# Kernel optimization log

Measured on AMD Instinct MI355X. Metric: run time of the kernel, lower is better.

The kernel has to match this reference:

```python
import jax, jax.numpy as jnp
import numpy as np
import math

D_MODEL = 1024
NUM_HEADS = 16
SEQ = 2048
BATCH = 4


def setup_inputs() -> dict:
    key = jax.random.key(0)
    ks = jax.random.split(key, 7)
    s = 0.02
    return {
        "x": jax.random.normal(ks[0], (BATCH, SEQ, D_MODEL), jnp.float32),
        "Wq": jax.random.normal(ks[1], (D_MODEL, D_MODEL), jnp.float32) * s,
        "bq": jax.random.normal(ks[2], (D_MODEL,), jnp.float32) * s,
        "Wkv": jax.random.normal(ks[3], (D_MODEL, 2 * D_MODEL), jnp.float32) * s,
        "bkv": jax.random.normal(ks[4], (2 * D_MODEL,), jnp.float32) * s,
        "Wo": jax.random.normal(ks[5], (D_MODEL, D_MODEL), jnp.float32) * s,
        "bo": jax.random.normal(ks[6], (D_MODEL,), jnp.float32) * s,
        "decoderMask": 1,
    }


def reference(x, Wq, bq, Wkv, bkv, Wo, bo, decoderMask):
    B, S, D = x.shape
    H = NUM_HEADS
    dh = D // H
    q_ = x @ Wq + bq              # [B,S,D]
    kv_ = x @ Wkv + bkv           # [B,S,2D] (self-attention: m is None)
    # Faithful to source: concat [q_, kv_] then reshape into heads of 3*dh,
    # which interleaves Q/KV projection columns across heads.
    qkv = jnp.concatenate([q_, kv_], axis=-1)          # [B,S,3D]
    qkv = qkv.reshape(B, S, H, 3 * dh).transpose(0, 2, 1, 3)  # [B,H,S,3dh]
    q, k, v = jnp.split(qkv, 3, axis=-1)               # each [B,H,S,dh]
    scaled = jnp.einsum("bhqd,bhkd->bhqk", q, k) / math.sqrt(dh)
    if decoderMask:
        mask = jnp.triu(jnp.full((S, S), -jnp.inf, dtype=scaled.dtype), k=1)
        scaled = scaled + mask
    attn = jax.nn.softmax(scaled, axis=-1)
    vals = jnp.einsum("bhqk,bhkd->bhqd", attn, v)      # [B,H,S,dh]
    vals = vals.transpose(0, 2, 1, 3).reshape(B, S, D)
    return vals @ Wo + bo
```

## Files before the change

kernel.cpp:

```cpp
#include <hip/hip_runtime.h>
#include <cstddef>
#include <cstdint>

#define SEQ   2048
#define BATCH 4
#define DM    1024
#define NH    16
#define DH    64
#define ROWS  (BATCH*SEQ)
#define NC3   3072
#define SM_SCALE 0.18033688f

typedef unsigned short u16;
typedef __attribute__((ext_vector_type(8))) short bf16x8;
typedef __attribute__((ext_vector_type(2))) float f32x2;
typedef __attribute__((ext_vector_type(4))) float f32x4;
typedef __attribute__((ext_vector_type(16))) float f32x16;
typedef __attribute__((ext_vector_type(4))) unsigned u32x4;
typedef __attribute__((ext_vector_type(2))) unsigned u32x2;

union V16 { f32x16 v; f32x2 p[8]; };

__device__ __forceinline__ u16 f2b(float f) {
  union { float f; unsigned u; } v; v.f = f;
  unsigned r = v.u + 0x7fffu + ((v.u >> 16) & 1u);
  return (u16)(r >> 16);
}

__device__ __forceinline__ unsigned cvt_pk_bf16(float lo, float hi) {
  unsigned r;
  asm("v_cvt_pk_bf16_f32 %0, %1, %2" : "=v"(r) : "v"(lo), "v"(hi));
  return r;
}

__device__ __forceinline__ void plswap(unsigned& a, unsigned& b) {
  auto rr = __builtin_amdgcn_permlane32_swap((int)a, (int)b, false, false);
  a = (unsigned)rr[0];
  b = (unsigned)rr[1];
}

__device__ __forceinline__ float ex2(float x) { return __builtin_amdgcn_exp2f(x); }

__device__ __forceinline__ void gld16(const void* g, void* l) {
  __builtin_amdgcn_global_load_lds((const __attribute__((address_space(1))) void*)g,
                                   (__attribute__((address_space(3))) void*)l,
                                   16, 0, 0);
}

__global__ __launch_bounds__(256) void prep_tw_kernel(
    const float* __restrict__ x, const float* __restrict__ bq,
    const float* __restrict__ bkv, u16* __restrict__ xb, float* __restrict__ bc,
    const float* __restrict__ Wq, const float* __restrict__ Wkv,
    const float* __restrict__ Wo, u16* __restrict__ Wt)
{
  __shared__ float t_[32][33];
  const int tid = threadIdx.x;
  if (blockIdx.x < 8192) {
    int i = blockIdx.x * 256 + tid;
    int idx = i * 4;
    float4 v = *(const float4*)(x + idx);
    xb[idx + 0] = f2b(v.x);
    xb[idx + 1] = f2b(v.y);
    xb[idx + 2] = f2b(v.z);
    xb[idx + 3] = f2b(v.w);
    if (i < NC3) bc[i] = (i < DM) ? bq[i] : bkv[i - DM];
  } else {
    const int bid = blockIdx.x - 8192;
    const int n0 = (bid & 127) * 32, k0 = (bid >> 7) * 32;
    const int xcol = tid & 31, yrow = tid >> 5;
    #pragma unroll
    for (int it = 0; it < 4; ++it) {
      int k = k0 + yrow + it * 8;
      int n = n0 + xcol;
      float v;
      if (n < DM)           v = Wq[k * DM + n];
      else if (n < NC3)     v = Wkv[k * (2 * DM) + (n - DM)];
      else                  v = Wo[k * DM + (n - NC3)];
      t_[yrow + it * 8][xcol] = v;
    }
    __syncthreads();
    #pragma unroll
    for (int it = 0; it < 4; ++it) {
      int n = n0 + yrow + it * 8;
      int k = k0 + xcol;
      Wt[(size_t)n * DM + k] = f2b(t_[xcol][yrow + it * 8]);
    }
  }
}

template <int MODE>
__global__ __launch_bounds__(256) void gemm_bt(
    const u16* __restrict__ A, const u16* __restrict__ Bt,
    const float* __restrict__ bias, void* __restrict__ C,
    u16* __restrict__ Vt, int M, int N, int K)
{
  __shared__ alignas(16) u16 lds_[4 * 8192];
  const int tid = threadIdx.x;
  const int lane = tid & 63, wid = tid >> 6;
  const int wr = (wid >> 1) * 64, wc = (wid & 1) * 64;
  const int l15 = lane & 15, lhi = lane >> 4;
  const int row0 = blockIdx.y * 128, col0 = blockIdx.x * 128;
  const int sr = tid >> 2, scol = (tid & 3) * 8;

  const u16* aS0 = A  + (size_t)(row0 + sr) * K + scol;
  const u16* aS1 = A  + (size_t)(row0 + 64 + sr) * K + scol;
  const u16* bS0 = Bt + (size_t)(col0 + sr) * K + scol;
  const u16* bS1 = Bt + (size_t)(col0 + 64 + sr) * K + scol;
  const int dA = tid * 8;

  int aoff[4], boff[4];
  #pragma unroll
  for (int m = 0; m < 4; ++m) aoff[m] = (wr + m * 16 + l15) * 32 + lhi * 8;
  #pragma unroll
  for (int n = 0; n < 4; ++n) boff[n] = 4096 + (wc + n * 16 + l15) * 32 + lhi * 8;

  f32x4 acc[4][4];
  #pragma unroll
  for (int m = 0; m < 4; ++m)
    #pragma unroll
    for (int n = 0; n < 4; ++n) { f32x4 z = {0.f, 0.f, 0.f, 0.f}; acc[m][n] = z; }

  const int KT = K >> 5;

  auto stage = [&](int kt) {
    u16* base = lds_ + (kt & 3) * 8192;
    const int ka = kt * 32;
    gld16(aS0 + ka, base + dA);
    gld16(aS1 + ka, base + 2048 + dA);
    gld16(bS0 + ka, base + 4096 + dA);
    gld16(bS1 + ka, base + 6144 + dA);
  };

  stage(0); stage(1); stage(2);
  asm volatile("s_waitcnt vmcnt(8)" ::: "memory");
  __builtin_amdgcn_s_barrier();

  for (int kt = 0; kt < KT; ++kt) {
    const u16* buf = lds_ + (kt & 3) * 8192;
    bf16x8 a[4], b[4];
    #pragma unroll
    for (int m = 0; m < 4; ++m) a[m] = *(const bf16x8*)&buf[aoff[m]];
    #pragma unroll
    for (int n = 0; n < 4; ++n) b[n] = *(const bf16x8*)&buf[boff[n]];
    if (kt + 3 < KT) stage(kt + 3);
    __builtin_amdgcn_s_setprio(1);
    #pragma unroll
    for (int m = 0; m < 4; ++m)
      #pragma unroll
      for (int n = 0; n < 4; ++n)
        acc[m][n] = __builtin_amdgcn_mfma_f32_16x16x32_bf16(a[m], b[n], acc[m][n], 0, 0, 0);
    __builtin_amdgcn_s_setprio(0);
    if (kt + 3 < KT)      { asm volatile("s_waitcnt vmcnt(8)" ::: "memory"); }
    else if (kt + 2 < KT) { asm volatile("s_waitcnt vmcnt(4)" ::: "memory"); }
    else if (kt + 1 < KT) { asm volatile("s_waitcnt vmcnt(0)" ::: "memory"); }
    __builtin_amdgcn_s_barrier();
  }

  #pragma unroll
  for (int m = 0; m < 4; ++m)
    #pragma unroll
    for (int n = 0; n < 4; ++n) {
      const int col = col0 + wc + n * 16 + l15;
      const float bv = bias[col];
      if (MODE == 0) {
        #pragma unroll
        for (int r = 0; r < 4; ++r) {
          const int row = row0 + wr + m * 16 + lhi * 4 + r;
          ((float*)C)[(size_t)row * N + col] = acc[m][n][r] + bv;
        }
      } else {
        const int hh = col / 192;
        const int cc = col - hh * 192;
        const float qs = (cc < 64) ? SM_SCALE : 1.f;
        u16 wv[4];
        #pragma unroll
        for (int r = 0; r < 4; ++r) {
          const int row = row0 + wr + m * 16 + lhi * 4 + r;
          wv[r] = f2b((acc[m][n][r] + bv) * qs);
          ((u16*)C)[(size_t)row * N + col] = wv[r];
        }
        if (cc >= 128) {
          const int row = row0 + wr + m * 16 + lhi * 4;
          const int bb = row >> 11, j = row & (SEQ - 1);
          u16* vt = Vt + ((size_t)(bb * NH + hh) * 64 + (cc - 128)) * SEQ + j;
          u32x2 pv = { (unsigned)wv[0] | ((unsigned)wv[1] << 16),
                       (unsigned)wv[2] | ((unsigned)wv[3] << 16) };
          *(u32x2*)vt = pv;
        }
      }
    }
}

__global__ __launch_bounds__(256) void attn_kernel(
    const u16* __restrict__ qkv, const u16* __restrict__ Vt, u16* __restrict__ ctx)
{
  const int bid = blockIdx.x;
  const int p   = (bid >> 3) & 7;
  const int g   = (bid & 7) + ((bid >> 6) << 3);
  const int h   = g & 15, b = g >> 4;
  const int tid = threadIdx.x;
  const int lane = tid & 63, wid = tid >> 6;
  const int l31 = lane & 31, lhi5 = lane >> 5;

  __shared__ alignas(16) u16 smem[4 * 64 * 64];

  const size_t kv_row = (size_t)(b * NH + h) * 64;
  const int sr = tid >> 3, sck = tid & 7;
  const int scks = sck ^ (sr & 7);

  const u16* kSrc0 = qkv + (size_t)(b * SEQ + sr) * NC3 + h * 192 + 64 + scks * 8;
  const u16* kSrc1 = kSrc0 + (size_t)32 * NC3;
  const u16* vSrc0 = Vt + (kv_row + sr) * SEQ + scks * 8;
  const u16* vSrc1 = vSrc0 + (size_t)32 * SEQ;
  const int dOff0 = sr * 64 + sck * 8;
  const int dOff1 = (32 + sr) * 64 + sck * 8;

  int koff[4], koff2[4];
  #pragma unroll
  for (int c = 0; c < 4; ++c) {
    koff[c]  = l31 * 64        + (((2 * c + lhi5) ^ (l31 & 7)) * 8);
    koff2[c] = (32 + l31) * 64 + (((2 * c + lhi5) ^ (l31 & 7)) * 8);
  }

  #pragma unroll 1
  for (int half = 0; half < 2; ++half) {
    const int qt = half ? (7 - p) : (8 + p);
    const int q0 = qt * 128;

    #pragma unroll
    for (int it = 0; it < 4; ++it) {
      int row = it * 32 + sr;
      gld16(qkv + (size_t)(b * SEQ + q0 + row) * NC3 + h * 192 + scks * 8,
            &smem[row * 64 + sck * 8]);
    }
    gld16(kSrc0, &smem[8192 + dOff0]);
    gld16(kSrc1, &smem[8192 + dOff1]);
    gld16(vSrc0, &smem[12288 + dOff0]);
    gld16(vSrc1, &smem[12288 + dOff1]);
    __syncthreads();

    bf16x8 qf[4];
    {
      const int qrow = wid * 32 + l31;
      #pragma unroll
      for (int c = 0; c < 4; ++c)
        qf[c] = *(const bf16x8*)&smem[qrow * 64 + (((2 * c + lhi5) ^ (qrow & 7)) * 8)];
    }
    __syncthreads();

    V16 o0, o1;
    #pragma unroll
    for (int r = 0; r < 16; ++r) { o0.v[r] = 0.f; o1.v[r] = 0.f; }
    float lrow = 0.f;

    const int nt = qt * 2 + 2;
    const int qw0 = q0 + wid * 32;
    const int qa  = qw0 + l31;
    const int dqb = qa - 4 * lhi5;

    for (int jt = 0; jt < nt; ++jt) {
      const int j0 = jt * 64;
      const u16* Kb = smem + ((jt & 1) ? 0 : 8192);
      const u16* Vb = smem + ((jt & 1) ? 4096 : 12288);

      if (jt + 1 < nt) {
        u16* Kn = smem + ((jt & 1) ? 8192 : 0);
        u16* Vn = smem + ((jt & 1) ? 12288 : 4096);
        const size_t kAdv = (size_t)(j0 + 64) * NC3;
        const int    vAdv = j0 + 64;
        gld16(kSrc0 + kAdv, &Kn[dOff0]);
        gld16(kSrc1 + kAdv, &Kn[dOff1]);
        gld16(vSrc0 + vAdv, &Vn[dOff0]);
        gld16(vSrc1 + vAdv, &Vn[dOff1]);
      }

      if (j0 <= qw0 + 31) {
        V16 s0, s1;
        #pragma unroll
        for (int r = 0; r < 16; ++r) { s0.v[r] = 0.f; s1.v[r] = 0.f; }
        __builtin_amdgcn_s_setprio(1);
        #pragma unroll
        for (int c = 0; c < 4; ++c) {
          bf16x8 kf = *(const bf16x8*)&Kb[koff[c]];
          s0.v = __builtin_amdgcn_mfma_f32_32x32x16_bf16(kf, qf[c], s0.v, 0, 0, 0);
        }
        #pragma unroll
        for (int c = 0; c < 4; ++c) {
          bf16x8 kf = *(const bf16x8*)&Kb[koff2[c]];
          s1.v = __builtin_amdgcn_mfma_f32_32x32x16_bf16(kf, qf[c], s1.v, 0, 0, 0);
        }
        __builtin_amdgcn_s_setprio(0);

        if (j0 + 63 > qw0) {
          const int dq = dqb - j0;
          #pragma unroll
          for (int r = 0; r < 16; ++r) {
            const int kvc = (r & 3) + 8 * (r >> 2);
            s0.v[r] = (kvc > dq)      ? -1e30f : s0.v[r];
            s1.v[r] = (kvc + 32 > dq) ? -1e30f : s1.v[r];
          }
        }

        f32x2 sum2 = {0.f, 0.f};
        #pragma unroll
        for (int i = 0; i < 8; ++i) {
          f32x2 e0, e1;
          e0[0] = ex2(s0.p[i][0]); e0[1] = ex2(s0.p[i][1]);
          e1[0] = ex2(s1.p[i][0]); e1[1] = ex2(s1.p[i][1]);
          s0.p[i] = e0; s1.p[i] = e1;
          sum2 += e0 + e1;
        }
        float ps = sum2[0] + sum2[1];
        {
          unsigned a = __builtin_bit_cast(unsigned, ps), bb = a;
          plswap(a, bb);
          ps = __builtin_bit_cast(float, a) + __builtin_bit_cast(float, bb);
        }
        lrow += ps;

        unsigned pk0[8], pk1[8];
        #pragma unroll
        for (int i = 0; i < 4; ++i) {
          pk0[2 * i]     = cvt_pk_bf16(s0.v[4 * i + 0], s0.v[4 * i + 1]);
          pk0[2 * i + 1] = cvt_pk_bf16(s0.v[4 * i + 2], s0.v[4 * i + 3]);
          pk1[2 * i]     = cvt_pk_bf16(s1.v[4 * i + 0], s1.v[4 * i + 1]);
          pk1[2 * i + 1] = cvt_pk_bf16(s1.v[4 * i + 2], s1.v[4 * i + 3]);
        }
        bf16x8 pf[4];
        {
          unsigned a0 = pk0[0], b0 = pk0[2]; plswap(a0, b0);
          unsigned a1 = pk0[1], b1 = pk0[3]; plswap(a1, b1);
          u32x4 w0v = {a0, a1, b0, b1}; pf[0] = __builtin_bit_cast(bf16x8, w0v);
          unsigned a2 = pk0[4], b2 = pk0[6]; plswap(a2, b2);
          unsigned a3 = pk0[5], b3 = pk0[7]; plswap(a3, b3);
          u32x4 w1v = {a2, a3, b2, b3}; pf[1] = __builtin_bit_cast(bf16x8, w1v);
          unsigned a4 = pk1[0], b4 = pk1[2]; plswap(a4, b4);
          unsigned a5 = pk1[1], b5 = pk1[3]; plswap(a5, b5);
          u32x4 w2v = {a4, a5, b4, b5}; pf[2] = __builtin_bit_cast(bf16x8, w2v);
          unsigned a6 = pk1[4], b6 = pk1[6]; plswap(a6, b6);
          unsigned a7 = pk1[5], b7 = pk1[7]; plswap(a7, b7);
          u32x4 w3v = {a6, a7, b6, b7}; pf[3] = __builtin_bit_cast(bf16x8, w3v);
        }

        __builtin_amdgcn_s_setprio(1);
        #pragma unroll
        for (int c = 0; c < 4; ++c) {
          bf16x8 vf = *(const bf16x8*)&Vb[koff[c]];
          o0.v = __builtin_amdgcn_mfma_f32_32x32x16_bf16(vf, pf[c], o0.v, 0, 0, 0);
        }
        #pragma unroll
        for (int c = 0; c < 4; ++c) {
          bf16x8 vf = *(const bf16x8*)&Vb[koff2[c]];
          o1.v = __builtin_amdgcn_mfma_f32_32x32x16_bf16(vf, pf[c], o1.v, 0, 0, 0);
        }
        __builtin_amdgcn_s_setprio(0);
      }
      __syncthreads();
    }

    const float inv = 1.f / lrow;
    u16* crow = ctx + (size_t)(b * SEQ + qa) * DM + h * DH;
    #pragma unroll
    for (int i = 0; i < 4; ++i) {
      u32x2 v0, v1;
      v0[0] = cvt_pk_bf16(o0.v[4 * i + 0] * inv, o0.v[4 * i + 1] * inv);
      v0[1] = cvt_pk_bf16(o0.v[4 * i + 2] * inv, o0.v[4 * i + 3] * inv);
      v1[0] = cvt_pk_bf16(o1.v[4 * i + 0] * inv, o1.v[4 * i + 1] * inv);
      v1[1] = cvt_pk_bf16(o1.v[4 * i + 2] * inv, o1.v[4 * i + 3] * inv);
      *(u32x2*)&crow[8 * i + 4 * lhi5]      = v0;
      *(u32x2*)&crow[32 + 8 * i + 4 * lhi5] = v1;
    }
  }
}

extern "C" void kernel_launch(void* const* d_in, const int* in_sizes, int n_in,
                              void* d_out, int out_size, void* d_ws, size_t ws_size,
                              hipStream_t stream) {
  (void)in_sizes; (void)n_in; (void)out_size; (void)ws_size;
  const float* x   = (const float*)d_in[0];
  const float* Wq  = (const float*)d_in[1];
  const float* bq  = (const float*)d_in[2];
  const float* Wkv = (const float*)d_in[3];
  const float* bkv = (const float*)d_in[4];
  const float* Wo  = (const float*)d_in[5];
  const float* bo  = (const float*)d_in[6];
  float* out = (float*)d_out;

  char* w = (char*)d_ws;
  size_t off = 0;
  auto alloc = [&](size_t bytes) { void* p = w + off; off += (bytes + 255) & ~(size_t)255; return p; };
  u16*   xb   = (u16*)alloc((size_t)ROWS * DM * 2);
  u16*   qkvb = (u16*)alloc((size_t)ROWS * NC3 * 2);
  u16*   Vt   = (u16*)alloc((size_t)BATCH * NH * DH * SEQ * 2);
  u16*   Wt   = (u16*)alloc((size_t)4096 * DM * 2);
  float* bc   = (float*)alloc((size_t)NC3 * 4);
  u16*   ctx  = xb;

  prep_tw_kernel<<<dim3(8192 + 4096), 256, 0, stream>>>(x, bq, bkv, xb, bc, Wq, Wkv, Wo, Wt);
  gemm_bt<1><<<dim3(NC3 / 128, ROWS / 128), 256, 0, stream>>>(xb, Wt, bc, qkvb, Vt, ROWS, NC3, DM);
  attn_kernel<<<dim3(512), 256, 0, stream>>>(qkvb, Vt, ctx);
  gemm_bt<0><<<dim3(DM / 128, ROWS / 128), 256, 0, stream>>>(ctx, Wt + (size_t)NC3 * DM, bo, out, nullptr, ROWS, DM, DM);
}
```

Before: 167.5 us.

## Swizzle GEMM tiles per XCD, use triple-buffered LDS, skip redundant V stores

```diff
diff --git a/kernel.cpp b/kernel.cpp
--- a/kernel.cpp
+++ b/kernel.cpp
@@ -94,12 +94,16 @@
     const float* __restrict__ bias, void* __restrict__ C,
     u16* __restrict__ Vt, int M, int N, int K)
 {
-  __shared__ alignas(16) u16 lds_[4 * 8192];
+  __shared__ alignas(16) u16 lds_[3 * 8192];
   const int tid = threadIdx.x;
   const int lane = tid & 63, wid = tid >> 6;
   const int wr = (wid >> 1) * 64, wc = (wid & 1) * 64;
   const int l15 = lane & 15, lhi = lane >> 4;
-  const int row0 = blockIdx.y * 128, col0 = blockIdx.x * 128;
+
+  const int bid = blockIdx.x;
+  const int xcd = bid & 7, t = bid >> 3;
+  const int rsub = t & 7, colb = t >> 3;
+  const int row0 = (xcd * 8 + rsub) * 128, col0 = colb * 128;
   const int sr = tid >> 2, scol = (tid & 3) * 8;
 
   const u16* aS0 = A  + (size_t)(row0 + sr) * K + scol;
@@ -122,8 +126,7 @@
 
   const int KT = K >> 5;
 
-  auto stage = [&](int kt) {
-    u16* base = lds_ + (kt & 3) * 8192;
+  auto stage = [&](int kt, u16* base) {
     const int ka = kt * 32;
     gld16(aS0 + ka, base + dA);
     gld16(aS1 + ka, base + 2048 + dA);
@@ -131,18 +134,23 @@
     gld16(bS1 + ka, base + 6144 + dA);
   };
 
-  stage(0); stage(1); stage(2);
-  asm volatile("s_waitcnt vmcnt(8)" ::: "memory");
+  u16* const bufA = lds_;
+  u16* const bufB = lds_ + 8192;
+  u16* const bufC = lds_ + 16384;
+
+  stage(0, bufA); stage(1, bufB);
+  asm volatile("s_waitcnt vmcnt(4)" ::: "memory");
   __builtin_amdgcn_s_barrier();
 
+  u16* rb = bufA;
+  u16* sb = bufC;
   for (int kt = 0; kt < KT; ++kt) {
-    const u16* buf = lds_ + (kt & 3) * 8192;
     bf16x8 a[4], b[4];
     #pragma unroll
-    for (int m = 0; m < 4; ++m) a[m] = *(const bf16x8*)&buf[aoff[m]];
-    #pragma unroll
-    for (int n = 0; n < 4; ++n) b[n] = *(const bf16x8*)&buf[boff[n]];
-    if (kt + 3 < KT) stage(kt + 3);
+    for (int m = 0; m < 4; ++m) a[m] = *(const bf16x8*)&rb[aoff[m]];
+    #pragma unroll
+    for (int n = 0; n < 4; ++n) b[n] = *(const bf16x8*)&rb[boff[n]];
+    if (kt + 2 < KT) stage(kt + 2, sb);
     __builtin_amdgcn_s_setprio(1);
     #pragma unroll
     for (int m = 0; m < 4; ++m)
@@ -150,10 +158,13 @@
       for (int n = 0; n < 4; ++n)
         acc[m][n] = __builtin_amdgcn_mfma_f32_16x16x32_bf16(a[m], b[n], acc[m][n], 0, 0, 0);
     __builtin_amdgcn_s_setprio(0);
-    if (kt + 3 < KT)      { asm volatile("s_waitcnt vmcnt(8)" ::: "memory"); }
-    else if (kt + 2 < KT) { asm volatile("s_waitcnt vmcnt(4)" ::: "memory"); }
-    else if (kt + 1 < KT) { asm volatile("s_waitcnt vmcnt(0)" ::: "memory"); }
-    __builtin_amdgcn_s_barrier();
+    if (kt + 1 < KT) {
+      if (kt + 2 < KT) { asm volatile("s_waitcnt vmcnt(4)" ::: "memory"); }
+      else             { asm volatile("s_waitcnt vmcnt(0)" ::: "memory"); }
+      __builtin_amdgcn_s_barrier();
+    }
+    rb = (rb == bufC) ? bufA : rb + 8192;
+    sb = (sb == bufC) ? bufA : sb + 8192;
   }
 
   #pragma unroll
@@ -171,15 +182,17 @@
       } else {
         const int hh = col / 192;
         const int cc = col - hh * 192;
-        const float qs = (cc < 64) ? SM_SCALE : 1.f;
-        u16 wv[4];
-        #pragma unroll
-        for (int r = 0; r < 4; ++r) {
-          const int row = row0 + wr + m * 16 + lhi * 4 + r;
-          wv[r] = f2b((acc[m][n][r] + bv) * qs);
-          ((u16*)C)[(size_t)row * N + col] = wv[r];
-        }
-        if (cc >= 128) {
+        if (cc < 128) {
+          const float qs = (cc < 64) ? SM_SCALE : 1.f;
+          #pragma unroll
+          for (int r = 0; r < 4; ++r) {
+            const int row = row0 + wr + m * 16 + lhi * 4 + r;
+            ((u16*)C)[(size_t)row * N + col] = f2b((acc[m][n][r] + bv) * qs);
+          }
+        } else {
+          u16 wv[4];
+          #pragma unroll
+          for (int r = 0; r < 4; ++r) wv[r] = f2b(acc[m][n][r] + bv);
           const int row = row0 + wr + m * 16 + lhi * 4;
           const int bb = row >> 11, j = row & (SEQ - 1);
           u16* vt = Vt + ((size_t)(bb * NH + hh) * 64 + (cc - 128)) * SEQ + j;
@@ -397,7 +410,7 @@
   u16*   ctx  = xb;
 
   prep_tw_kernel<<<dim3(8192 + 4096), 256, 0, stream>>>(x, bq, bkv, xb, bc, Wq, Wkv, Wo, Wt);
-  gemm_bt<1><<<dim3(NC3 / 128, ROWS / 128), 256, 0, stream>>>(xb, Wt, bc, qkvb, Vt, ROWS, NC3, DM);
+  gemm_bt<1><<<dim3((ROWS / 128) * (NC3 / 128)), 256, 0, stream>>>(xb, Wt, bc, qkvb, Vt, ROWS, NC3, DM);
   attn_kernel<<<dim3(512), 256, 0, stream>>>(qkvb, Vt, ctx);
-  gemm_bt<0><<<dim3(DM / 128, ROWS / 128), 256, 0, stream>>>(ctx, Wt + (size_t)NC3 * DM, bo, out, nullptr, ROWS, DM, DM);
-}
+  gemm_bt<0><<<dim3((ROWS / 128) * (DM / 128)), 256, 0, stream>>>(ctx, Wt + (size_t)NC3 * DM, bo, out, nullptr, ROWS, DM, DM);
+}
```

Result: faster. 161.6 us (-3.5%).
